# Kernel optimization log

Hardware: AMD Instinct MI355X
Metric: run time of the kernel (lower is better)

Reference implementation:

```python
import jax, jax.numpy as jnp
from jax import lax
import numpy as np

N_QUBITS = 10  # min(dim, n_wires) wires carry RX gates; rest stay |0>


def setup_inputs() -> dict:
    key = jax.random.key(0)
    k1, k2, k3, k4 = jax.random.split(key, 4)
    T, B, D, H, C = 128, 512, 512, 512, 32
    inputs = jax.random.normal(k1, (T, B, D), dtype=jnp.float32)
    # 4 gates (f, i, g, o), centres init ~ 0.1 * randn as in the module
    centres = 0.1 * jax.random.normal(k2, (4, C, D + H), dtype=jnp.float32)
    lin_w = jax.random.normal(k3, (4, H, C), dtype=jnp.float32) / jnp.sqrt(jnp.float32(C))
    lin_b = jax.random.normal(k4, (4, H), dtype=jnp.float32) * 0.01
    return {"inputs": inputs, "centres": centres, "lin_w": lin_w, "lin_b": lin_b}


def _quantum_kernel(comb, ctr):
    # comb: [B, dim], ctr: [C, dim]
    # Circuit = RX(x_i) then RX(-y_i) on wire i (i < N_QUBITS) => RX(x_i - y_i).
    # |<0..0|state>| = prod_i |cos((x_i - y_i)/2)| over active wires.
    m = min(comb.shape[-1], N_QUBITS)
    diff = comb[:, None, :m] - ctr[None, :, :m]  # [B, C, m]
    return jnp.prod(jnp.abs(jnp.cos(0.5 * diff)), axis=-1)  # [B, C]


def reference(inputs, centres, lin_w, lin_b):
    T, B, D = inputs.shape
    H = lin_w.shape[1]
    h0 = jnp.zeros((B, H), dtype=inputs.dtype)
    c0 = jnp.zeros((B, H), dtype=inputs.dtype)

    def step(carry, x):
        h, c = carry
        comb = jnp.concatenate([x, h], axis=1)  # [B, D+H]
        # kernels for all 4 gates at once: [4, B, C]
        k = jax.vmap(lambda ct: _quantum_kernel(comb, ct))(centres)
        pre = jnp.einsum('gbc,ghc->gbh', k, lin_w) + lin_b[:, None, :]  # [4, B, H]
        f = jax.nn.sigmoid(pre[0])
        i = jax.nn.sigmoid(pre[1])
        g = jnp.tanh(pre[2])
        o = jax.nn.sigmoid(pre[3])
        c_new = f * c + i * g
        h_new = o * jnp.tanh(c_new)
        return (h_new, c_new), h_new

    (h, c), outputs = lax.scan(step, (h0, c0), inputs)
    return outputs, h, c
```

## Files before the change

kernel.cpp:

```cpp
#include <hip/hip_runtime.h>

#define TT 128
#define BB 512
#define DD 512
#define HH 512
#define CC 32
#define NQ 10
#define GC 128
#define DH 1024
#define CHUNK 8
#define NCHUNK (TT / CHUNK)
#define L2E 1.4426950408889634f

typedef __fp16 h2 __attribute__((ext_vector_type(2)));
typedef __fp16 h4 __attribute__((ext_vector_type(4)));
typedef __fp16 h8 __attribute__((ext_vector_type(8)));
typedef float f4 __attribute__((ext_vector_type(4)));

__device__ __forceinline__ float rcpf(float x) {
    return __builtin_amdgcn_rcpf(x);
}
__device__ __forceinline__ float exp2fast(float x) {
#if __has_builtin(__builtin_amdgcn_exp2f)
    return __builtin_amdgcn_exp2f(x);
#else
    return exp2f(x);
#endif
}

__global__ __launch_bounds__(512, 2) void qlstm_kernel(
    const float* __restrict__ inputs,
    const float* __restrict__ centres,
    const float* __restrict__ lin_w,
    const float* __restrict__ lin_b,
    float* __restrict__ out)
{
    __shared__ __fp16 Klds[TT * GC];
    __shared__ uint2  preB[CHUNK * HH];
    __shared__ float xs[TT * 12];
    __shared__ float cs[GC * 12];

    const int b = blockIdx.x;
    const int tid = threadIdx.x;
    const int lane = tid & 63;
    const int w = tid >> 6;
    const int q = lane >> 4;
    const int c16 = lane & 15;

    h8 bfr[16];
    {
        const int c0 = q * 8;
        #pragma unroll
        for (int g = 0; g < 4; ++g) {
            const float s = (g == 2) ? (2.f * L2E) : (-L2E);
            #pragma unroll
            for (int j = 0; j < 4; ++j) {
                const int hcol = (w * 4 + j) * 16 + c16;
                const float* wp = lin_w + (((size_t)g * HH + hcol) * CC + c0);
                f4 lo = *(const f4*)wp;
                f4 hi = *(const f4*)(wp + 4);
                h2 p0 = __builtin_amdgcn_cvt_pkrtz(s * lo.x, s * lo.y);
                h2 p1 = __builtin_amdgcn_cvt_pkrtz(s * lo.z, s * lo.w);
                h2 p2 = __builtin_amdgcn_cvt_pkrtz(s * hi.x, s * hi.y);
                h2 p3 = __builtin_amdgcn_cvt_pkrtz(s * hi.z, s * hi.w);
                h8 bb = { p0.x, p0.y, p1.x, p1.y, p2.x, p2.y, p3.x, p3.y };
                bfr[g * 4 + j] = bb;
            }
        }
    }

    const float bias0 = -L2E * lin_b[0 * HH + tid];
    const float bias1 = -L2E * lin_b[1 * HH + tid];
    const float bias2 = 2.f * L2E * lin_b[2 * HH + tid];
    const float bias3 = -L2E * lin_b[3 * HH + tid];

    for (int idx = tid; idx < TT * NQ; idx += 512) {
        int t = idx / NQ, qq = idx - t * NQ;
        xs[t * 12 + qq] = 0.5f * inputs[((size_t)t * BB + b) * DD + qq];
    }
    for (int idx = tid; idx < GC * NQ; idx += 512) {
        int gc = idx / NQ, qq = idx - gc * NQ;
        cs[gc * 12 + qq] = 0.5f * centres[(size_t)gc * DH + qq];
    }
    __syncthreads();

    {
        const int gcq = (tid & 31) * 4;
        const int t0 = tid >> 5;
        #pragma unroll
        for (int p = 0; p < 8; ++p) {
            const int t = t0 + p * 16;
            const f4* xrow = (const f4*)&xs[t * 12];
            f4 x0 = xrow[0], x1 = xrow[1], x2 = xrow[2];
            float pv[4];
            #pragma unroll
            for (int u = 0; u < 4; ++u) {
                const f4* crow = (const f4*)&cs[(gcq + u) * 12];
                f4 cA = crow[0], cB = crow[1], cD = crow[2];
                float pr;
                pr  = fabsf(__cosf(x0.x - cA.x));
                pr *= fabsf(__cosf(x0.y - cA.y));
                pr *= fabsf(__cosf(x0.z - cA.z));
                pr *= fabsf(__cosf(x0.w - cA.w));
                pr *= fabsf(__cosf(x1.x - cB.x));
                pr *= fabsf(__cosf(x1.y - cB.y));
                pr *= fabsf(__cosf(x1.z - cB.z));
                pr *= fabsf(__cosf(x1.w - cB.w));
                pr *= fabsf(__cosf(x2.x - cD.x));
                pr *= fabsf(__cosf(x2.y - cD.y));
                pv[u] = pr;
            }
            h2 lo2 = __builtin_amdgcn_cvt_pkrtz(pv[0], pv[1]);
            h2 hi2 = __builtin_amdgcn_cvt_pkrtz(pv[2], pv[3]);
            h4 kk = { lo2.x, lo2.y, hi2.x, hi2.y };
            int byteo = (t * 256 + gcq * 2) ^ ((t & 7) << 4);
            *(h4*)((char*)Klds + byteo) = kk;
        }
    }
    __syncthreads();

    float cstate = 0.f, hstate = 0.f;
    float* op = out + (size_t)b * HH + tid;
    const int tlo = c16 & 7;
    const f4 z4 = {0.f, 0.f, 0.f, 0.f};
    int aoff[4];
    #pragma unroll
    for (int g = 0; g < 4; ++g)
        aoff[g] = tlo * 256 + ((g * 64 + q * 16) ^ (tlo << 4));

    for (int ct = 0; ct < NCHUNK; ++ct) {
        const char* arp = (const char*)Klds + ct * 2048;
        h8 afr[4];
        #pragma unroll
        for (int g = 0; g < 4; ++g)
            afr[g] = *(const h8*)(arp + aoff[g]);

        #pragma unroll
        for (int j = 0; j < 4; ++j) {
            f4 a0 = __builtin_amdgcn_mfma_f32_16x16x32_f16(afr[0], bfr[0*4+j], z4, 0, 0, 0);
            f4 a1 = __builtin_amdgcn_mfma_f32_16x16x32_f16(afr[1], bfr[1*4+j], z4, 0, 0, 0);
            f4 a2 = __builtin_amdgcn_mfma_f32_16x16x32_f16(afr[2], bfr[2*4+j], z4, 0, 0, 0);
            f4 a3 = __builtin_amdgcn_mfma_f32_16x16x32_f16(afr[3], bfr[3*4+j], z4, 0, 0, 0);
            if (q < 2) {
                const int hcol = (w * 4 + j) * 16 + c16;
                #pragma unroll
                for (int r = 0; r < 4; ++r) {
                    const int tl = q * 4 + r;
                    h2 p01 = __builtin_amdgcn_cvt_pkrtz(a0[r], a1[r]);
                    h2 p23 = __builtin_amdgcn_cvt_pkrtz(a2[r], a3[r]);
                    uint2 uu;
                    uu.x = *(unsigned*)&p01;
                    uu.y = *(unsigned*)&p23;
                    preB[tl * HH + hcol] = uu;
                }
            }
        }

        #pragma unroll
        for (int tl = 0; tl < CHUNK; ++tl) {
            uint2 vv = preB[tl * HH + tid];
            h2 vfi = *(h2*)&vv.x;
            h2 vgo = *(h2*)&vv.y;
            float yf = bias0 + (float)vfi.x;
            float yi = bias1 + (float)vfi.y;
            float yg = bias2 + (float)vgo.x;
            float yo = bias3 + (float)vgo.y;
            float fg = rcpf(1.f + exp2fast(yf));
            float ig = rcpf(1.f + exp2fast(yi));
            float og = rcpf(1.f + exp2fast(yo));
            float gg = 1.f - 2.f * rcpf(1.f + exp2fast(yg));
            cstate = fg * cstate + ig * gg;
            float th = 1.f - 2.f * rcpf(1.f + exp2fast((2.f * L2E) * cstate));
            hstate = og * th;
            op[(size_t)(ct * CHUNK + tl) * (BB * HH)] = hstate;
        }
    }

    float* hout = out + (size_t)TT * BB * HH;
    float* cout = hout + (size_t)BB * HH;
    hout[(size_t)b * HH + tid] = hstate;
    cout[(size_t)b * HH + tid] = cstate;
}

extern "C" void kernel_launch(void* const* d_in, const int* in_sizes, int n_in,
                              void* d_out, int out_size, void* d_ws, size_t ws_size,
                              hipStream_t stream) {
    const float* inputs  = (const float*)d_in[0];
    const float* centres = (const float*)d_in[1];
    const float* lin_w   = (const float*)d_in[2];
    const float* lin_b   = (const float*)d_in[3];
    float* out = (float*)d_out;

    qlstm_kernel<<<dim3(BB), dim3(512), 0, stream>>>(inputs, centres, lin_w, lin_b, out);
}
```

Measured before the change: 84.56 us.

## Fold bias into MFMA accumulator and move gate activations before the LDS handoff

The bias is now loaded into the MFMA accumulator init, so the pre-activation arrives already biased. The sigmoid/tanh gate nonlinearities are computed right after the MFMA by the writing lanes, and a compact (forget-gate fp32, i*g and o as fp16) tuple goes through LDS. The sequential recurrence then only does the cell fma and one tanh, with the cell state kept pre-scaled by 2*log2(e) and rescaled at the end. The x and centre staging is moved into the preB region with a transposed centre layout, and the kernel-product loop is restructured to save LDS. This trims the serial per-step work and LDS footprint, but concentrates transcendental work on half the lanes (q<2) and adds fp16 rounding of i*g.

```diff
diff --git a/kernel.cpp b/kernel.cpp
--- a/kernel.cpp
+++ b/kernel.cpp
@@ -17,9 +17,7 @@
 typedef __fp16 h8 __attribute__((ext_vector_type(8)));
 typedef float f4 __attribute__((ext_vector_type(4)));
 
-__device__ __forceinline__ float rcpf(float x) {
-    return __builtin_amdgcn_rcpf(x);
-}
+__device__ __forceinline__ float rcpf(float x) { return __builtin_amdgcn_rcpf(x); }
 __device__ __forceinline__ float exp2fast(float x) {
 #if __has_builtin(__builtin_amdgcn_exp2f)
     return __builtin_amdgcn_exp2f(x);
@@ -36,9 +34,11 @@
     float* __restrict__ out)
 {
     __shared__ __fp16 Klds[TT * GC];
-    __shared__ uint2  preB[CHUNK * HH];
-    __shared__ float xs[TT * 12];
-    __shared__ float cs[GC * 12];
+    __shared__ __align__(16) uint2 preB[8 * HH];
+    __shared__ float blds[4 * HH];
+
+    float* csT = (float*)preB;
+    float* xsA = (float*)preB + NQ * 128;
 
     const int b = blockIdx.x;
     const int tid = threadIdx.x;
@@ -46,6 +46,21 @@
     const int w = tid >> 6;
     const int q = lane >> 4;
     const int c16 = lane & 15;
+
+    for (int idx = tid; idx < TT * NQ; idx += 512) {
+        int t = idx / NQ, d = idx - t * NQ;
+        xsA[t * 12 + d] = 0.5f * inputs[((size_t)t * BB + b) * DD + d];
+    }
+    for (int idx = tid; idx < GC * NQ; idx += 512) {
+        int gc = idx & 127, d = idx >> 7;
+        csT[d * 128 + gc] = 0.5f * centres[(size_t)gc * DH + d];
+    }
+    for (int idx = tid; idx < 4 * HH; idx += 512) {
+        int g = idx >> 9;
+        float s = (g == 2) ? (2.f * L2E) : (-L2E);
+        blds[idx] = s * lin_b[idx];
+    }
+    __syncthreads();
 
     h8 bfr[16];
     {
@@ -69,49 +84,24 @@
         }
     }
 
-    const float bias0 = -L2E * lin_b[0 * HH + tid];
-    const float bias1 = -L2E * lin_b[1 * HH + tid];
-    const float bias2 = 2.f * L2E * lin_b[2 * HH + tid];
-    const float bias3 = -L2E * lin_b[3 * HH + tid];
-
-    for (int idx = tid; idx < TT * NQ; idx += 512) {
-        int t = idx / NQ, qq = idx - t * NQ;
-        xs[t * 12 + qq] = 0.5f * inputs[((size_t)t * BB + b) * DD + qq];
-    }
-    for (int idx = tid; idx < GC * NQ; idx += 512) {
-        int gc = idx / NQ, qq = idx - gc * NQ;
-        cs[gc * 12 + qq] = 0.5f * centres[(size_t)gc * DH + qq];
-    }
-    __syncthreads();
-
     {
         const int gcq = (tid & 31) * 4;
         const int t0 = tid >> 5;
         #pragma unroll
         for (int p = 0; p < 8; ++p) {
             const int t = t0 + p * 16;
-            const f4* xrow = (const f4*)&xs[t * 12];
-            f4 x0 = xrow[0], x1 = xrow[1], x2 = xrow[2];
-            float pv[4];
+            float pr0 = 1.f, pr1 = 1.f, pr2 = 1.f, pr3 = 1.f;
             #pragma unroll
-            for (int u = 0; u < 4; ++u) {
-                const f4* crow = (const f4*)&cs[(gcq + u) * 12];
-                f4 cA = crow[0], cB = crow[1], cD = crow[2];
-                float pr;
-                pr  = fabsf(__cosf(x0.x - cA.x));
-                pr *= fabsf(__cosf(x0.y - cA.y));
-                pr *= fabsf(__cosf(x0.z - cA.z));
-                pr *= fabsf(__cosf(x0.w - cA.w));
-                pr *= fabsf(__cosf(x1.x - cB.x));
-                pr *= fabsf(__cosf(x1.y - cB.y));
-                pr *= fabsf(__cosf(x1.z - cB.z));
-                pr *= fabsf(__cosf(x1.w - cB.w));
-                pr *= fabsf(__cosf(x2.x - cD.x));
-                pr *= fabsf(__cosf(x2.y - cD.y));
-                pv[u] = pr;
+            for (int d = 0; d < NQ; ++d) {
+                float xd = xsA[t * 12 + d];
+                f4 cd = *(const f4*)&csT[d * 128 + gcq];
+                pr0 *= fabsf(__cosf(xd - cd.x));
+                pr1 *= fabsf(__cosf(xd - cd.y));
+                pr2 *= fabsf(__cosf(xd - cd.z));
+                pr3 *= fabsf(__cosf(xd - cd.w));
             }
-            h2 lo2 = __builtin_amdgcn_cvt_pkrtz(pv[0], pv[1]);
-            h2 hi2 = __builtin_amdgcn_cvt_pkrtz(pv[2], pv[3]);
+            h2 lo2 = __builtin_amdgcn_cvt_pkrtz(pr0, pr1);
+            h2 hi2 = __builtin_amdgcn_cvt_pkrtz(pr2, pr3);
             h4 kk = { lo2.x, lo2.y, hi2.x, hi2.y };
             int byteo = (t * 256 + gcq * 2) ^ ((t & 7) << 4);
             *(h4*)((char*)Klds + byteo) = kk;
@@ -119,14 +109,14 @@
     }
     __syncthreads();
 
-    float cstate = 0.f, hstate = 0.f;
+    float cs2 = 0.f, hstate = 0.f;
     float* op = out + (size_t)b * HH + tid;
     const int tlo = c16 & 7;
-    const f4 z4 = {0.f, 0.f, 0.f, 0.f};
     int aoff[4];
     #pragma unroll
     for (int g = 0; g < 4; ++g)
         aoff[g] = tlo * 256 + ((g * 64 + q * 16) ^ (tlo << 4));
+    const int hcolbase = w * 64 + c16;
 
     for (int ct = 0; ct < NCHUNK; ++ct) {
         const char* arp = (const char*)Klds + ct * 2048;
@@ -137,49 +127,52 @@
 
         #pragma unroll
         for (int j = 0; j < 4; ++j) {
-            f4 a0 = __builtin_amdgcn_mfma_f32_16x16x32_f16(afr[0], bfr[0*4+j], z4, 0, 0, 0);
-            f4 a1 = __builtin_amdgcn_mfma_f32_16x16x32_f16(afr[1], bfr[1*4+j], z4, 0, 0, 0);
-            f4 a2 = __builtin_amdgcn_mfma_f32_16x16x32_f16(afr[2], bfr[2*4+j], z4, 0, 0, 0);
-            f4 a3 = __builtin_amdgcn_mfma_f32_16x16x32_f16(afr[3], bfr[3*4+j], z4, 0, 0, 0);
+            const int hcol = hcolbase + j * 16;
+            const float bf = blds[0 * HH + hcol];
+            const float bi = blds[1 * HH + hcol];
+            const float bg = blds[2 * HH + hcol];
+            const float bo = blds[3 * HH + hcol];
+            f4 cf = { bf, bf, bf, bf };
+            f4 ci = { bi, bi, bi, bi };
+            f4 cg = { bg, bg, bg, bg };
+            f4 co = { bo, bo, bo, bo };
+            f4 aF = __builtin_amdgcn_mfma_f32_16x16x32_f16(afr[0], bfr[0*4+j], cf, 0, 0, 0);
+            f4 aI = __builtin_amdgcn_mfma_f32_16x16x32_f16(afr[1], bfr[1*4+j], ci, 0, 0, 0);
+            f4 aG = __builtin_amdgcn_mfma_f32_16x16x32_f16(afr[2], bfr[2*4+j], cg, 0, 0, 0);
+            f4 aO = __builtin_amdgcn_mfma_f32_16x16x32_f16(afr[3], bfr[3*4+j], co, 0, 0, 0);
             if (q < 2) {
-                const int hcol = (w * 4 + j) * 16 + c16;
                 #pragma unroll
                 for (int r = 0; r < 4; ++r) {
-                    const int tl = q * 4 + r;
-                    h2 p01 = __builtin_amdgcn_cvt_pkrtz(a0[r], a1[r]);
-                    h2 p23 = __builtin_amdgcn_cvt_pkrtz(a2[r], a3[r]);
+                    float F   = rcpf(1.f + exp2fast(aF[r]));
+                    float si  = rcpf(1.f + exp2fast(aI[r]));
+                    float rg  = rcpf(1.f + exp2fast(aG[r]));
+                    float gg2 = fmaf(-4.f * L2E, rg, 2.f * L2E);
+                    float O   = rcpf(1.f + exp2fast(aO[r]));
+                    h2 io = __builtin_amdgcn_cvt_pkrtz(si * gg2, O);
                     uint2 uu;
-                    uu.x = *(unsigned*)&p01;
-                    uu.y = *(unsigned*)&p23;
-                    preB[tl * HH + hcol] = uu;
+                    uu.x = __builtin_bit_cast(unsigned, F);
+                    uu.y = *(unsigned*)&io;
+                    preB[(q * 4 + r) * HH + hcol] = uu;
                 }
             }
         }
 
         #pragma unroll
-        for (int tl = 0; tl < CHUNK; ++tl) {
-            uint2 vv = preB[tl * HH + tid];
-            h2 vfi = *(h2*)&vv.x;
-            h2 vgo = *(h2*)&vv.y;
-            float yf = bias0 + (float)vfi.x;
-            float yi = bias1 + (float)vfi.y;
-            float yg = bias2 + (float)vgo.x;
-            float yo = bias3 + (float)vgo.y;
-            float fg = rcpf(1.f + exp2fast(yf));
-            float ig = rcpf(1.f + exp2fast(yi));
-            float og = rcpf(1.f + exp2fast(yo));
-            float gg = 1.f - 2.f * rcpf(1.f + exp2fast(yg));
-            cstate = fg * cstate + ig * gg;
-            float th = 1.f - 2.f * rcpf(1.f + exp2fast((2.f * L2E) * cstate));
-            hstate = og * th;
-            op[(size_t)(ct * CHUNK + tl) * (BB * HH)] = hstate;
+        for (int s = 0; s < CHUNK; ++s) {
+            uint2 vv = preB[s * HH + tid];
+            float F = __builtin_bit_cast(float, vv.x);
+            h2 io = *(h2*)&vv.y;
+            cs2 = fmaf(F, cs2, (float)io.x);
+            float th = fmaf(-2.f, rcpf(1.f + exp2fast(cs2)), 1.f);
+            hstate = (float)io.y * th;
+            op[(size_t)(ct * CHUNK + s) * (BB * HH)] = hstate;
         }
     }
 
     float* hout = out + (size_t)TT * BB * HH;
     float* cout = hout + (size_t)BB * HH;
     hout[(size_t)b * HH + tid] = hstate;
-    cout[(size_t)b * HH + tid] = cstate;
+    cout[(size_t)b * HH + tid] = cs2 * 0.34657359027997264f;
 }
 
 extern "C" void kernel_launch(void* const* d_in, const int* in_sizes, int n_in,
```

Result: slower. 101.5 us (+20.0%).
